# Kernel tuning notes

Hardware: AMD Instinct MI355X
Metric: run time of the kernel (lower is better)

The kernel has to match this reference:

```python
import jax, jax.numpy as jnp
import numpy as np

EMBED = 1024
HEADS = 16
HEAD_DIM = EMBED // HEADS


def setup_inputs() -> dict:
    key = jax.random.key(0)
    ks = jax.random.split(key, 9)
    N, L = 2, 2048
    inp = {
        "values": jax.random.normal(ks[0], (N, L, EMBED), dtype=jnp.float32),
        "keys": jax.random.normal(ks[1], (N, L, EMBED), dtype=jnp.float32),
        "query": jax.random.normal(ks[2], (N, L, EMBED), dtype=jnp.float32),
        "mask": jax.random.randint(ks[3], (N, 1, L, L), 0, 2, dtype=jnp.int32),
        # per-head projection weights (torch Linear: y = x @ W.T), bias=False
        "Wv": jax.random.normal(ks[4], (HEAD_DIM, HEAD_DIM), dtype=jnp.float32) / np.sqrt(HEAD_DIM),
        "Wk": jax.random.normal(ks[5], (HEAD_DIM, HEAD_DIM), dtype=jnp.float32) / np.sqrt(HEAD_DIM),
        "Wq": jax.random.normal(ks[6], (HEAD_DIM, HEAD_DIM), dtype=jnp.float32) / np.sqrt(HEAD_DIM),
        "Wo": jax.random.normal(ks[7], (EMBED, EMBED), dtype=jnp.float32) / np.sqrt(EMBED),
        "bo": jax.random.normal(ks[8], (EMBED,), dtype=jnp.float32) * 0.02,
    }
    return inp


def reference(values, keys, query, mask, Wv, Wk, Wq, Wo, bo):
    N, Lq = query.shape[0], query.shape[1]
    Lk = keys.shape[1]
    # reshape to (N, L, H, D)
    v = values.reshape(N, Lk, HEADS, HEAD_DIM)
    k = keys.reshape(N, Lk, HEADS, HEAD_DIM)
    q = query.reshape(N, Lq, HEADS, HEAD_DIM)
    # per-head_dim linear projections (shared across heads): x @ W.T
    v = jnp.einsum('nlhd,ed->nlhe', v, Wv)
    k = jnp.einsum('nlhd,ed->nlhe', k, Wk)
    q = jnp.einsum('nqhd,ed->nqhe', q, Wq)
    # scores [N, H, Lq, Lk]
    energy = jnp.einsum('nqhd,nkhd->nhqk', q, k) / np.sqrt(HEAD_DIM).astype(np.float32)
    energy = jnp.where(mask == 0, jnp.float32(-1e20), energy)
    attn = jax.nn.softmax(energy, axis=-1)
    out = jnp.einsum('nhql,nlhd->nqhd', attn, v).reshape(N, Lq, EMBED)
    return out @ Wo.T + bo
```

## Files before the change

### kernel.cpp

```cpp
#include <hip/hip_runtime.h>
#include <hip/hip_bf16.h>

#define SEQ 2048
#define NH 16
#define DH 64
#define EMB 1024

typedef __bf16 bf16;
typedef __attribute__((ext_vector_type(8))) __bf16 bf16x8;
typedef __attribute__((ext_vector_type(4))) __bf16 bf16x4;
typedef __attribute__((ext_vector_type(4))) float f32x4;
typedef __attribute__((ext_vector_type(4))) unsigned int u32x4;
typedef unsigned long long u64;

#define OFF_MQK  0
#define OFF_WO2  8192
#define OFF_K2   (8192 + 2097152)
#define OFF_VT   (OFF_K2 + 8388608)
#define OFF_A2   (OFF_VT + 8388608)
#define OFF_MB   (OFF_A2 + 8388608)

#define LOG2E 1.44269504088896340736f

__device__ __forceinline__ f32x4 mfma16(bf16x8 a, bf16x8 b, f32x4 c) {
  return __builtin_amdgcn_mfma_f32_16x16x32_bf16(a, b, c, 0, 0, 0);
}

#define GL16(g, l)                                                            \
  __builtin_amdgcn_global_load_lds(                                           \
      (const __attribute__((address_space(1))) void*)(g),                     \
      (__attribute__((address_space(3))) void*)(l), 16, 0, 0)

__device__ __forceinline__ unsigned pack_bf16(float p0, float p1) {
  unsigned short b0 = __builtin_bit_cast(unsigned short, (bf16)p0);
  unsigned short b1 = __builtin_bit_cast(unsigned short, (bf16)p1);
  return (unsigned)b0 | ((unsigned)b1 << 16);
}

__global__ __launch_bounds__(256) void prep0(const float* __restrict__ Wq,
                                             const float* __restrict__ Wk,
                                             bf16* __restrict__ mqk) {
  __shared__ float wq[64 * 64];
  __shared__ float wk[64 * 64];
  int tid = threadIdx.x;
  for (int i = tid; i < 4096; i += 256) { wq[i] = Wq[i]; wk[i] = Wk[i]; }
  __syncthreads();
  for (int idx = tid; idx < 4096; idx += 256) {
    int d1 = idx >> 6, d2 = idx & 63;
    float s = 0.f;
#pragma unroll
    for (int e = 0; e < 64; ++e) s += wq[e * 64 + d1] * wk[e * 64 + d2];
    mqk[idx] = (bf16)(s * 0.125f * LOG2E);
  }
}

__global__ __launch_bounds__(256) void prep_fused(
    const float* __restrict__ Wo, const float* __restrict__ Wv,
    const float* __restrict__ keys, const bf16* __restrict__ mqk,
    const float* __restrict__ values, const int* __restrict__ mask,
    bf16* __restrict__ wo2f, bf16* __restrict__ k2f, bf16* __restrict__ vtf,
    u64* __restrict__ mbt) {
  __shared__ __align__(16) float smem[5184];
  int blk = blockIdx.x;
  int tid = threadIdx.x;

  if (blk < 1024) {
    int e = blk;
    float* wv = smem;
    float* worow = smem + 4096;
    for (int i = tid; i < 4096; i += 256) wv[i] = Wv[i];
    for (int i = tid; i < 1024; i += 256) worow[i] = Wo[(size_t)e * 1024 + i];
    __syncthreads();
    int c0 = tid * 4;
    bf16x4 w;
#pragma unroll
    for (int j = 0; j < 4; ++j) {
      int col = c0 + j;
      int hb = col & ~63, dp = col & 63;
      float s = 0.f;
#pragma unroll
      for (int d = 0; d < 64; ++d) s += worow[hb + d] * wv[d * 64 + dp];
      w[j] = (bf16)s;
    }
    int et = e >> 6, t = (e >> 4) & 3, cc = e & 15;
    int kc = c0 >> 5, gg = (c0 >> 3) & 3, half = (c0 >> 2) & 1;
    char* dst = (char*)wo2f + ((size_t)(et * 32 + kc)) * 4096 + t * 1024 +
                (gg * 16 + cc) * 16 + 8 * half;
    *(bf16x4*)dst = w;
  } else if (blk < 2048) {
    int b = blk - 1024;
    int lt = b & 31, h = (b >> 5) & 15, n = b >> 9;
    int wave = tid >> 6, lane = tid & 63;
    int g = lane >> 4, c = lane & 15;
    bf16x8 am[4][2];
#pragma unroll
    for (int t = 0; t < 4; ++t)
#pragma unroll
      for (int s = 0; s < 2; ++s)
        am[t][s] = *(const bf16x8*)(mqk + (16 * t + c) * 64 + 32 * s + 8 * g);
    int l = lt * 64 + wave * 16 + c;
    const float* krow = keys + ((size_t)(n * SEQ + l)) * EMB + h * DH;
    bf16x8 bfr[2];
#pragma unroll
    for (int s = 0; s < 2; ++s) {
      f32x4 x0 = *(const f32x4*)(krow + 32 * s + 8 * g);
      f32x4 x1 = *(const f32x4*)(krow + 32 * s + 8 * g + 4);
      bf16x8 t;
#pragma unroll
      for (int i = 0; i < 4; ++i) { t[i] = (bf16)x0[i]; t[4 + i] = (bf16)x1[i]; }
      bfr[s] = t;
    }
    char* tb = (char*)k2f + (size_t)((n * NH + h) * 32 + lt) * 8192 + wave * 2048;
#pragma unroll
    for (int t = 0; t < 4; ++t) {
      f32x4 a = {0.f, 0.f, 0.f, 0.f};
      a = mfma16(am[t][0], bfr[0], a);
      a = mfma16(am[t][1], bfr[1], a);
      bf16x4 w;
#pragma unroll
      for (int r = 0; r < 4; ++r) w[r] = (bf16)a[r];
      char* dst = tb + (t >> 1) * 1024 +
                  ((2 * (t & 1) + (g >> 1)) * 16 + c) * 16 + 8 * (g & 1);
      *(bf16x4*)dst = w;
    }
  } else if (blk < 3072) {
    int b = blk - 2048;
    int lt = b & 31, h = (b >> 5) & 15, n = b >> 9;
    float (*lds)[65] = (float(*)[65])smem;
    {
      int r = tid >> 2, cg = (tid & 3) * 16;
      const float* vrow =
          values + ((size_t)(n * SEQ + lt * 64 + r)) * EMB + h * DH + cg;
#pragma unroll
      for (int j = 0; j < 16; j += 4) {
        f32x4 x = *(const f32x4*)(vrow + j);
        lds[r][cg + j + 0] = x[0];
        lds[r][cg + j + 1] = x[1];
        lds[r][cg + j + 2] = x[2];
        lds[r][cg + j + 3] = x[3];
      }
    }
    __syncthreads();
    {
      int d = tid >> 2, q16 = tid & 3, lb = q16 * 16;
      bf16x8 w0, w1;
#pragma unroll
      for (int j = 0; j < 8; ++j) w0[j] = (bf16)lds[lb + j][d];
#pragma unroll
      for (int j = 0; j < 8; ++j) w1[j] = (bf16)lds[lb + 8 + j][d];
      int dt = d >> 4, cc = d & 15;
      int s = q16 >> 1, gg = 2 * (q16 & 1);
      char* base = (char*)vtf + (size_t)((n * NH + h) * 32 + lt) * 8192 +
                   (2 * dt + s) * 1024;
      *(bf16x8*)(base + (gg * 16 + cc) * 16) = w0;
      *(bf16x8*)(base + ((gg + 1) * 16 + cc) * 16) = w1;
    }
  } else {
    int base = (blk - 3072) * 4 + (tid >> 6);
    int lane = tid & 63;
#pragma unroll
    for (int i = 0; i < 16; ++i) {
      int w = base + i * 8192;
      int v = mask[(size_t)w * 64 + lane];
      u64 bbits = __ballot(v != 0);
      int kw = w & 31, q = (w >> 5) & 2047, nn = w >> 16;
      if (lane == 0) mbt[((size_t)nn * 32 + kw) * 2048 + q] = bbits;
    }
  }
}

__global__ __launch_bounds__(64, 2) void attn(const float* __restrict__ qraw,
                                              const bf16* __restrict__ k2f,
                                              const bf16* __restrict__ vtf,
                                              const u64* __restrict__ mbt,
                                              bf16* __restrict__ a2) {
  int swz = ((blockIdx.x & 7) << 8) | (blockIdx.x >> 3);
  int qt = swz & 63, h = (swz >> 6) & 15, n = swz >> 10;
  int lane = threadIdx.x, g = lane >> 4, c = lane & 15;

  __shared__ u64 lutm[16];
  if (lane < 16) {
    unsigned a = (lane & 1 ? 0xFFFFu : 0u) | (lane & 2 ? 0xFFFF0000u : 0u);
    unsigned b = (lane & 4 ? 0xFFFFu : 0u) | (lane & 8 ? 0xFFFF0000u : 0u);
    lutm[lane] = (u64)a | ((u64)b << 32);
  }
  __syncthreads();

  bf16x8 qf[2][2];
#pragma unroll
  for (int qi = 0; qi < 2; ++qi) {
    int q = qt * 32 + qi * 16 + c;
    const float* qrow = qraw + ((size_t)(n * SEQ + q)) * EMB + h * DH;
#pragma unroll
    for (int s = 0; s < 2; ++s) {
      f32x4 x0 = *(const f32x4*)(qrow + 32 * s + 8 * g);
      f32x4 x1 = *(const f32x4*)(qrow + 32 * s + 8 * g + 4);
      bf16x8 t;
#pragma unroll
      for (int i = 0; i < 4; ++i) { t[i] = (bf16)x0[i]; t[4 + i] = (bf16)x1[i]; }
      qf[qi][s] = t;
    }
  }
  const char* kp = (const char*)k2f + (size_t)(n * NH + h) * 32 * 8192 + lane * 16;
  const char* vp = (const char*)vtf + (size_t)(n * NH + h) * 32 * 8192 + lane * 16;
  const u64* mq = mbt + (size_t)n * 32 * 2048 + qt * 32 + c;

  bf16x8 K[8], Vv[8];
#pragma unroll
  for (int j = 0; j < 8; ++j) K[j] = *(const bf16x8*)(kp + j * 1024);

  f32x4 oacc[2][4];
#pragma unroll
  for (int qi = 0; qi < 2; ++qi)
#pragma unroll
    for (int dt = 0; dt < 4; ++dt) oacc[qi][dt] = (f32x4){0.f, 0.f, 0.f, 0.f};
  float mrun[2] = {-1e30f, -1e30f}, lrun[2] = {0.f, 0.f};
  bf16x8 ones;
#pragma unroll
  for (int i = 0; i < 8; ++i) ones[i] = (bf16)1.0f;
  int sh0 = 4 * g, sh1 = sh0 + 16;
  int srcA = ((g & 1) << 5) | c;
  int srcB = srcA + 16;
  bool hi2 = (g >> 1) != 0;

  for (int kt = 0; kt < 32; ++kt) {
#pragma unroll
    for (int j = 0; j < 8; ++j)
      Vv[j] = *(const bf16x8*)(vp + (size_t)kt * 8192 + j * 1024);
    u64 mw0 = mq[kt * 2048];
    u64 mw1 = mq[kt * 2048 + 16];

    f32x4 sacc[2][4];
#pragma unroll
    for (int t = 0; t < 4; ++t) {
      bf16x8 k0 = K[2 * t], k1 = K[2 * t + 1];
#pragma unroll
      for (int qi = 0; qi < 2; ++qi) {
        f32x4 a = {0.f, 0.f, 0.f, 0.f};
        a = mfma16(k0, qf[qi][0], a);
        a = mfma16(k1, qf[qi][1], a);
        sacc[qi][t] = a;
      }
    }
#pragma unroll
    for (int j = 0; j < 8; ++j)
      K[j] = *(const bf16x8*)(kp + (size_t)(kt + 1) * 8192 + j * 1024);

    float tmax[2];
#pragma unroll
    for (int qi = 0; qi < 2; ++qi) {
      float x0 = sacc[qi][0][0], x1 = sacc[qi][0][1], x2 = sacc[qi][0][2],
            x3 = sacc[qi][0][3], x4 = sacc[qi][1][0], x5 = sacc[qi][1][1],
            x6 = sacc[qi][1][2], x7 = sacc[qi][1][3], x8 = sacc[qi][2][0],
            x9 = sacc[qi][2][1], xa = sacc[qi][2][2], xb = sacc[qi][2][3],
            xc = sacc[qi][3][0], xd = sacc[qi][3][1], xe = sacc[qi][3][2],
            xf = sacc[qi][3][3];
      float t0 = fmaxf(fmaxf(x0, x1), x2);
      float t1 = fmaxf(fmaxf(x3, x4), x5);
      float t2 = fmaxf(fmaxf(x6, x7), x8);
      float t3 = fmaxf(fmaxf(x9, xa), xb);
      float t4 = fmaxf(fmaxf(xc, xd), xe);
      float m = fmaxf(fmaxf(fmaxf(t0, t1), t2), fmaxf(fmaxf(t3, t4), xf));
      m = fmaxf(m, __shfl_xor(m, 16));
      m = fmaxf(m, __shfl_xor(m, 32));
      tmax[qi] = m;
    }
    bool needs = (tmax[0] > mrun[0] + 8.f) || (tmax[1] > mrun[1] + 8.f);
    if (__any(needs)) {
#pragma unroll
      for (int qi = 0; qi < 2; ++qi) {
        float mnew = fmaxf(mrun[qi], tmax[qi]);
        float scl = __builtin_amdgcn_exp2f(mrun[qi] - mnew);
        lrun[qi] *= scl;
#pragma unroll
        for (int dt = 0; dt < 4; ++dt) {
          oacc[qi][dt][0] *= scl; oacc[qi][dt][1] *= scl;
          oacc[qi][dt][2] *= scl; oacc[qi][dt][3] *= scl;
        }
        mrun[qi] = mnew;
      }
    }
    unsigned wpk[2][4][2];
    u64 mwa[2] = {mw0, mw1};
#pragma unroll
    for (int qi = 0; qi < 2; ++qi) {
      unsigned mlo = (unsigned)mwa[qi], mhi = (unsigned)(mwa[qi] >> 32);
      u64 L[4];
      L[0] = lutm[(mlo >> sh0) & 15];
      L[1] = lutm[(mlo >> sh1) & 15];
      L[2] = lutm[(mhi >> sh0) & 15];
      L[3] = lutm[(mhi >> sh1) & 15];
      float mr = mrun[qi];
#pragma unroll
      for (int t = 0; t < 4; ++t) {
        float p0 = __builtin_amdgcn_exp2f(sacc[qi][t][0] - mr);
        float p1 = __builtin_amdgcn_exp2f(sacc[qi][t][1] - mr);
        float p2 = __builtin_amdgcn_exp2f(sacc[qi][t][2] - mr);
        float p3 = __builtin_amdgcn_exp2f(sacc[qi][t][3] - mr);
        wpk[qi][t][0] = pack_bf16(p0, p1) & (unsigned)L[t];
        wpk[qi][t][1] = pack_bf16(p2, p3) & (unsigned)(L[t] >> 32);
      }
    }
    bf16x8 pf[2][2];
#pragma unroll
    for (int qi = 0; qi < 2; ++qi)
#pragma unroll
      for (int s = 0; s < 2; ++s) {
        unsigned ta0 = (unsigned)__shfl((int)wpk[qi][2 * s][0], srcA);
        unsigned ta1 = (unsigned)__shfl((int)wpk[qi][2 * s][1], srcA);
        unsigned tb0 = (unsigned)__shfl((int)wpk[qi][2 * s + 1][0], srcA);
        unsigned tb1 = (unsigned)__shfl((int)wpk[qi][2 * s + 1][1], srcA);
        unsigned ua0 = (unsigned)__shfl((int)wpk[qi][2 * s][0], srcB);
        unsigned ua1 = (unsigned)__shfl((int)wpk[qi][2 * s][1], srcB);
        unsigned ub0 = (unsigned)__shfl((int)wpk[qi][2 * s + 1][0], srcB);
        unsigned ub1 = (unsigned)__shfl((int)wpk[qi][2 * s + 1][1], srcB);
        u32x4 f;
        f[0] = hi2 ? tb0 : ta0;
        f[1] = hi2 ? tb1 : ta1;
        f[2] = hi2 ? ub0 : ua0;
        f[3] = hi2 ? ub1 : ua1;
        pf[qi][s] = __builtin_bit_cast(bf16x8, f);
      }
    f32x4 pacc[2];
#pragma unroll
    for (int qi = 0; qi < 2; ++qi) {
      f32x4 a = {0.f, 0.f, 0.f, 0.f};
      a = mfma16(ones, pf[qi][0], a);
      a = mfma16(ones, pf[qi][1], a);
      pacc[qi] = a;
    }
#pragma unroll
    for (int dt = 0; dt < 4; ++dt)
#pragma unroll
      for (int s = 0; s < 2; ++s) {
        bf16x8 vf = Vv[2 * dt + s];
#pragma unroll
        for (int qi = 0; qi < 2; ++qi)
          oacc[qi][dt] = mfma16(vf, pf[qi][s], oacc[qi][dt]);
      }
#pragma unroll
    for (int qi = 0; qi < 2; ++qi) lrun[qi] += pacc[qi][0];
  }
#pragma unroll
  for (int qi = 0; qi < 2; ++qi) {
    float inv = 1.0f / lrun[qi];
    int q = qt * 32 + qi * 16 + c;
    bf16* orow = a2 + ((size_t)(n * SEQ + q)) * EMB + h * DH;
#pragma unroll
    for (int dt = 0; dt < 4; ++dt) {
      bf16x4 w2;
#pragma unroll
      for (int r = 0; r < 4; ++r) w2[r] = (bf16)(oacc[qi][dt][r] * inv);
      *(bf16x4*)(orow + 16 * dt + 4 * g) = w2;
    }
  }
}

__global__ __launch_bounds__(256) void out_gemm(const bf16* __restrict__ a2,
                                                const bf16* __restrict__ wo2f,
                                                const float* __restrict__ bo,
                                                float* __restrict__ out) {
  int blk = blockIdx.x;
  int et = blk & 15, mt = blk >> 4;
  int tid = threadIdx.x, wave = tid >> 6, lane = tid & 63;
  int g = lane >> 4, c = lane & 15;
  int m = mt * 64 + wave * 16 + c;
  const bf16* arow = a2 + (size_t)m * EMB + 8 * g;

  __shared__ bf16 wbuf[2][4096];
  const char* wtile = (const char*)wo2f + (size_t)et * 32 * 4096;
  int lofs = lane * 16, wofs = wave * 1024;

#define STAGEW(J, BUF)                                                        \
  {                                                                           \
    const char* src_ = wtile + (size_t)(J) * 8192 + wofs + lofs;              \
    char* dst_ = (char*)&wbuf[BUF][0] + wofs;                                 \
    GL16(src_, dst_);                                                         \
    GL16(src_ + 4096, dst_ + 4096);                                           \
  }

  STAGEW(0, 0);
  bf16x8 bn0 = *(const bf16x8*)(arow);
  bf16x8 bn1 = *(const bf16x8*)(arow + 32);
  __syncthreads();

  f32x4 acc[4];
#pragma unroll
  for (int t = 0; t < 4; ++t) acc[t] = (f32x4){0.f, 0.f, 0.f, 0.f};

  for (int j = 0; j < 16; ++j) {
    int cur = j & 1;
    bf16x8 b0 = bn0, b1 = bn1;
    if (j < 15) {
      STAGEW(j + 1, cur ^ 1);
      bn0 = *(const bf16x8*)(arow + (j + 1) * 64);
      bn1 = *(const bf16x8*)(arow + (j + 1) * 64 + 32);
    }
    const bf16* wb = &wbuf[cur][0];
#pragma unroll
    for (int t = 0; t < 4; ++t)
      acc[t] = mfma16(*(const bf16x8*)(wb + t * 512 + lane * 8), b0, acc[t]);
#pragma unroll
    for (int t = 0; t < 4; ++t)
      acc[t] =
          mfma16(*(const bf16x8*)(wb + 2048 + t * 512 + lane * 8), b1, acc[t]);
    __syncthreads();
  }
#pragma unroll
  for (int t = 0; t < 4; ++t) {
    int e = et * 64 + 16 * t + 4 * g;
    f32x4 b = *(const f32x4*)(bo + e);
    f32x4 w;
#pragma unroll
    for (int r = 0; r < 4; ++r) w[r] = acc[t][r] + b[r];
    *(f32x4*)(out + (size_t)m * EMB + e) = w;
  }
}

extern "C" void kernel_launch(void* const* d_in, const int* in_sizes, int n_in,
                              void* d_out, int out_size, void* d_ws, size_t ws_size,
                              hipStream_t stream) {
  const float* values = (const float*)d_in[0];
  const float* keys   = (const float*)d_in[1];
  const float* query  = (const float*)d_in[2];
  const int*   mask   = (const int*)d_in[3];
  const float* Wv     = (const float*)d_in[4];
  const float* Wk     = (const float*)d_in[5];
  const float* Wq     = (const float*)d_in[6];
  const float* Wo     = (const float*)d_in[7];
  const float* bo     = (const float*)d_in[8];

  char* ws = (char*)d_ws;
  bf16* mqk  = (bf16*)(ws + OFF_MQK);
  bf16* wo2f = (bf16*)(ws + OFF_WO2);
  bf16* k2f  = (bf16*)(ws + OFF_K2);
  bf16* vtf  = (bf16*)(ws + OFF_VT);
  bf16* a2   = (bf16*)(ws + OFF_A2);
  u64*  mbt  = (u64*)(ws + OFF_MB);

  prep0<<<1, 256, 0, stream>>>(Wq, Wk, mqk);
  prep_fused<<<5120, 256, 0, stream>>>(Wo, Wv, keys, mqk, values, mask,
                                       wo2f, k2f, vtf, mbt);
  attn<<<2048, 64, 0, stream>>>(query, k2f, vtf, mbt, a2);
  out_gemm<<<1024, 256, 0, stream>>>(a2, wo2f, bo, (float*)d_out);
}
```

Measured before the change: 126.1 us.

## Split attention key range across two waves with LDS softmax merge

The attention kernel now runs two waves per block, each covering half of the key tiles with its own online-softmax state. At the end the partial max, sum and output accumulators of the second wave are passed through LDS, and the first wave rescales and merges them before writing. This doubles the number of waves in flight to hide memory and MFMA latency, at the cost of a block barrier, LDS traffic and a merge step. The tiny Wq·Wk prep kernel is also spread from one block to sixteen.

Result: slower. 284.4 us (+125.4%).

```diff
diff --git a/kernel.cpp b/kernel.cpp
--- a/kernel.cpp
+++ b/kernel.cpp
@@ -42,16 +42,14 @@
                                              bf16* __restrict__ mqk) {
   __shared__ float wq[64 * 64];
   __shared__ float wk[64 * 64];
-  int tid = threadIdx.x;
+  int tid = threadIdx.x, b = blockIdx.x;
   for (int i = tid; i < 4096; i += 256) { wq[i] = Wq[i]; wk[i] = Wk[i]; }
   __syncthreads();
-  for (int idx = tid; idx < 4096; idx += 256) {
-    int d1 = idx >> 6, d2 = idx & 63;
-    float s = 0.f;
-#pragma unroll
-    for (int e = 0; e < 64; ++e) s += wq[e * 64 + d1] * wk[e * 64 + d2];
-    mqk[idx] = (bf16)(s * 0.125f * LOG2E);
-  }
+  int d1 = b * 4 + (tid >> 6), d2 = tid & 63;
+  float s = 0.f;
+#pragma unroll
+  for (int e = 0; e < 64; ++e) s += wq[e * 64 + d1] * wk[e * 64 + d2];
+  mqk[d1 * 64 + d2] = (bf16)(s * 0.125f * LOG2E);
 }
 
 __global__ __launch_bounds__(256) void prep_fused(
@@ -169,20 +167,23 @@
   }
 }
 
-__global__ __launch_bounds__(64, 2) void attn(const float* __restrict__ qraw,
-                                              const bf16* __restrict__ k2f,
-                                              const bf16* __restrict__ vtf,
-                                              const u64* __restrict__ mbt,
-                                              bf16* __restrict__ a2) {
+__global__ __launch_bounds__(128, 4) void attn(const float* __restrict__ qraw,
+                                               const bf16* __restrict__ k2f,
+                                               const bf16* __restrict__ vtf,
+                                               const u64* __restrict__ mbt,
+                                               bf16* __restrict__ a2) {
   int swz = ((blockIdx.x & 7) << 8) | (blockIdx.x >> 3);
   int qt = swz & 63, h = (swz >> 6) & 15, n = swz >> 10;
-  int lane = threadIdx.x, g = lane >> 4, c = lane & 15;
+  int tid = threadIdx.x, wave = tid >> 6, lane = tid & 63;
+  int g = lane >> 4, c = lane & 15;
 
   __shared__ u64 lutm[16];
-  if (lane < 16) {
-    unsigned a = (lane & 1 ? 0xFFFFu : 0u) | (lane & 2 ? 0xFFFF0000u : 0u);
-    unsigned b = (lane & 4 ? 0xFFFFu : 0u) | (lane & 8 ? 0xFFFF0000u : 0u);
-    lutm[lane] = (u64)a | ((u64)b << 32);
+  __shared__ f32x4 lds_o[8][64];
+  __shared__ float lds_m[2][16], lds_l[2][16];
+  if (tid < 16) {
+    unsigned a = (tid & 1 ? 0xFFFFu : 0u) | (tid & 2 ? 0xFFFF0000u : 0u);
+    unsigned b = (tid & 4 ? 0xFFFFu : 0u) | (tid & 8 ? 0xFFFF0000u : 0u);
+    lutm[tid] = (u64)a | ((u64)b << 32);
   }
   __syncthreads();
 
@@ -205,9 +206,12 @@
   const char* vp = (const char*)vtf + (size_t)(n * NH + h) * 32 * 8192 + lane * 16;
   const u64* mq = mbt + (size_t)n * 32 * 2048 + qt * 32 + c;
 
+  int kt0 = wave * 16;
+
   bf16x8 K[8], Vv[8];
 #pragma unroll
-  for (int j = 0; j < 8; ++j) K[j] = *(const bf16x8*)(kp + j * 1024);
+  for (int j = 0; j < 8; ++j)
+    K[j] = *(const bf16x8*)(kp + (size_t)kt0 * 8192 + j * 1024);
 
   f32x4 oacc[2][4];
 #pragma unroll
@@ -223,7 +227,7 @@
   int srcB = srcA + 16;
   bool hi2 = (g >> 1) != 0;
 
-  for (int kt = 0; kt < 32; ++kt) {
+  for (int kt = kt0; kt < kt0 + 16; ++kt) {
 #pragma unroll
     for (int j = 0; j < 8; ++j)
       Vv[j] = *(const bf16x8*)(vp + (size_t)kt * 8192 + j * 1024);
@@ -341,17 +345,38 @@
 #pragma unroll
     for (int qi = 0; qi < 2; ++qi) lrun[qi] += pacc[qi][0];
   }
-#pragma unroll
-  for (int qi = 0; qi < 2; ++qi) {
-    float inv = 1.0f / lrun[qi];
-    int q = qt * 32 + qi * 16 + c;
-    bf16* orow = a2 + ((size_t)(n * SEQ + q)) * EMB + h * DH;
-#pragma unroll
-    for (int dt = 0; dt < 4; ++dt) {
-      bf16x4 w2;
-#pragma unroll
-      for (int r = 0; r < 4; ++r) w2[r] = (bf16)(oacc[qi][dt][r] * inv);
-      *(bf16x4*)(orow + 16 * dt + 4 * g) = w2;
+
+  if (wave == 1) {
+#pragma unroll
+    for (int qi = 0; qi < 2; ++qi) {
+#pragma unroll
+      for (int dt = 0; dt < 4; ++dt) lds_o[qi * 4 + dt][lane] = oacc[qi][dt];
+      if (g == 0) {
+        lds_m[qi][c] = mrun[qi];
+        lds_l[qi][c] = lrun[qi];
+      }
+    }
+  }
+  __syncthreads();
+  if (wave == 0) {
+#pragma unroll
+    for (int qi = 0; qi < 2; ++qi) {
+      float mB = lds_m[qi][c], lB = lds_l[qi][c];
+      float ms = fmaxf(mrun[qi], mB);
+      float sA = __builtin_amdgcn_exp2f(mrun[qi] - ms);
+      float sB = __builtin_amdgcn_exp2f(mB - ms);
+      float inv = 1.0f / (lrun[qi] * sA + lB * sB);
+      int q = qt * 32 + qi * 16 + c;
+      bf16* orow = a2 + ((size_t)(n * SEQ + q)) * EMB + h * DH;
+#pragma unroll
+      for (int dt = 0; dt < 4; ++dt) {
+        f32x4 ob = lds_o[qi * 4 + dt][lane];
+        bf16x4 w2;
+#pragma unroll
+        for (int r = 0; r < 4; ++r)
+          w2[r] = (bf16)((oacc[qi][dt][r] * sA + ob[r] * sB) * inv);
+        *(bf16x4*)(orow + 16 * dt + 4 * g) = w2;
+      }
     }
   }
 }
@@ -438,9 +463,9 @@
   bf16* a2   = (bf16*)(ws + OFF_A2);
   u64*  mbt  = (u64*)(ws + OFF_MB);
 
-  prep0<<<1, 256, 0, stream>>>(Wq, Wk, mqk);
+  prep0<<<16, 256, 0, stream>>>(Wq, Wk, mqk);
   prep_fused<<<5120, 256, 0, stream>>>(Wo, Wv, keys, mqk, values, mask,
                                        wo2f, k2f, vtf, mbt);
-  attn<<<2048, 64, 0, stream>>>(query, k2f, vtf, mbt, a2);
+  attn<<<2048, 128, 0, stream>>>(query, k2f, vtf, mbt, a2);
   out_gemm<<<1024, 256, 0, stream>>>(a2, wo2f, bo, (float*)d_out);
 }
```
